# Optimization experiments

Hardware: AMD Instinct MI355X
Metric: run time of the kernel (lower is better)

## Reference

```python
import jax, jax.numpy as jnp
import numpy as np

B, N, DIM = 8, 4096, 512
HEADS, DHEAD = 8, 64
HIDDEN = HEADS * DHEAD  # 512
COND = 512
EPS = 1e-5


def layer_norm(x, gamma, beta):
    mu = jnp.mean(x, axis=-1, keepdims=True)
    var = jnp.var(x, axis=-1, keepdims=True)
    return (x - mu) * jax.lax.rsqrt(var + EPS) * gamma + beta


def setup_inputs() -> dict:
    key = jax.random.key(0)
    ks = jax.random.split(key, 8)
    s_in = 1.0 / np.sqrt(DIM)
    s_cond = 1.0 / np.sqrt(COND)
    s_hid = 1.0 / np.sqrt(HIDDEN)
    return {
        "x": jax.random.normal(ks[0], (B, N, DIM), jnp.float32),
        "conditioning_embeddings": jax.random.normal(ks[1], (B, COND), jnp.float32),
        "gamma_in": jnp.ones((DIM,), jnp.float32),
        "w_cond": jax.random.normal(ks[2], (2 * DIM, COND), jnp.float32) * s_cond,
        "b_cond": jax.random.normal(ks[3], (2 * DIM,), jnp.float32) * 0.01,
        "w_qkv": jax.random.normal(ks[4], (3 * HIDDEN, DIM), jnp.float32) * s_in,
        "w_out": jax.random.normal(ks[5], (DIM, HIDDEN), jnp.float32) * s_hid,
        "gamma_out": jnp.ones((DIM,), jnp.float32),
    }


def reference(x, conditioning_embeddings, gamma_in, w_cond, b_cond, w_qkv, w_out, gamma_out):
    scale_f = DHEAD ** (-0.5)
    # pre-norm
    x = layer_norm(x, gamma_in, jnp.zeros_like(gamma_in))
    # conditioning affine: SiLU -> Linear -> broadcast over tokens
    cond = jax.nn.silu(conditioning_embeddings) @ w_cond.T + b_cond  # [b, 2*dim]
    scale, shift = jnp.split(cond, 2, axis=-1)
    x = x * (scale[:, None, :] + 1.0) + shift[:, None, :]
    # qkv projection (no bias)
    qkv = x @ w_qkv.T  # [b, n, 3*hidden]
    q, k, v = jnp.split(qkv, 3, axis=-1)
    def to_heads(t):
        return t.reshape(B, N, HEADS, DHEAD).transpose(0, 2, 1, 3)  # b h n d
    q, k, v = to_heads(q), to_heads(k), to_heads(v)
    q = jax.nn.softmax(q, axis=-1) * scale_f  # softmax over feature dim
    k = jax.nn.softmax(k, axis=-2)            # softmax over sequence dim
    context = jnp.einsum('bhnd,bhne->bhde', k, v)
    out = jnp.einsum('bhde,bhnd->bhne', context, q)
    out = out.transpose(0, 2, 1, 3).reshape(B, N, HIDDEN)  # b n (h d)
    out = out @ w_out.T
    return layer_norm(out, gamma_out, jnp.zeros_like(gamma_out))
```

## Files before the change

kernel.cpp:

```cpp
#include <hip/hip_runtime.h>
#include <hip/hip_bf16.h>
#include <math.h>

typedef unsigned short u16;
typedef __attribute__((ext_vector_type(4))) float f32x4;
typedef __attribute__((ext_vector_type(8))) short s16x8;

#define B_    8
#define N_    4096
#define DIM_  512
#define TOK   32768
#define QKVD  1536

__device__ __forceinline__ float bf2f(u16 u) {
    union { unsigned int i; float f; } x; x.i = ((unsigned int)u) << 16; return x.f;
}
__device__ __forceinline__ u16 f2bf(float f) {
    union { float f; unsigned int i; } x; x.f = f;
    unsigned int r = (x.i + 0x7fffu + ((x.i >> 16) & 1u)) >> 16;
    return (u16)r;
}

__device__ __forceinline__ void gload_lds16(const void* g, void* l) {
    __builtin_amdgcn_global_load_lds(
        (const __attribute__((address_space(1))) unsigned int*)g,
        (__attribute__((address_space(3))) unsigned int*)l, 16, 0, 0);
}

__device__ __forceinline__ int swz8(int row, int p) { return p ^ (row & 7); }

__global__ void k_cond(const float* __restrict__ ce, const float* __restrict__ w_cond,
                       const float* __restrict__ b_cond, float* __restrict__ cond)
{
    __shared__ float s[512];
    int jt = blockIdx.x, b = blockIdx.y;
    int tid = threadIdx.x, wid = tid >> 6, lane = tid & 63;
    for (int i = tid; i < 512; i += 256) {
        float v = ce[b * 512 + i];
        s[i] = v / (1.f + __expf(-v));
    }
    __syncthreads();
#pragma unroll
    for (int jj = 0; jj < 4; ++jj) {
        int j = jt * 16 + wid * 4 + jj;
        const float4* w4 = (const float4*)(w_cond + (size_t)j * 512);
        float4 a = w4[lane * 2], c = w4[lane * 2 + 1];
        float acc = a.x*s[lane*8+0] + a.y*s[lane*8+1] + a.z*s[lane*8+2] + a.w*s[lane*8+3]
                  + c.x*s[lane*8+4] + c.y*s[lane*8+5] + c.z*s[lane*8+6] + c.w*s[lane*8+7];
#pragma unroll
        for (int d = 1; d < 64; d <<= 1) acc += __shfl_xor(acc, d, 64);
        if (lane == 0) cond[b * 1024 + j] = acc + b_cond[j];
    }
}

__global__ void k_w2bf(const float* __restrict__ w, u16* __restrict__ wb)
{
    int i = (blockIdx.x * 256 + threadIdx.x) * 4;
    float4 v = *(const float4*)&w[i];
    ushort4 o; o.x = f2bf(v.x); o.y = f2bf(v.y); o.z = f2bf(v.z); o.w = f2bf(v.w);
    *(ushort4*)&wb[i] = o;
}

__global__ void k_lnmod(const float* __restrict__ x, const float* __restrict__ cond,
                        const float* __restrict__ gamma, u16* __restrict__ xm)
{
    int wave = threadIdx.x >> 6, lane = threadIdx.x & 63;
    size_t t = (size_t)blockIdx.x * 4 + wave;
    const float* xr = x + t * 512;
    float4 v0 = ((const float4*)xr)[lane * 2];
    float4 v1 = ((const float4*)xr)[lane * 2 + 1];
    float s  = v0.x+v0.y+v0.z+v0.w + v1.x+v1.y+v1.z+v1.w;
    float ss = v0.x*v0.x+v0.y*v0.y+v0.z*v0.z+v0.w*v0.w
             + v1.x*v1.x+v1.y*v1.y+v1.z*v1.z+v1.w*v1.w;
#pragma unroll
    for (int m = 1; m < 64; m <<= 1) { s += __shfl_xor(s, m, 64); ss += __shfl_xor(ss, m, 64); }
    float mu = s * (1.f/512.f);
    float var = ss * (1.f/512.f) - mu * mu;
    float rs = rsqrtf(var + 1e-5f);
    int b = (int)(t >> 12);
    const float* cb = cond + b * 1024;
    float4 g0  = ((const float4*)gamma)[lane*2],     g1  = ((const float4*)gamma)[lane*2+1];
    float4 sc0 = ((const float4*)cb)[lane*2],        sc1 = ((const float4*)cb)[lane*2+1];
    float4 sh0 = ((const float4*)(cb+512))[lane*2],  sh1 = ((const float4*)(cb+512))[lane*2+1];
    ushort4 o0, o1;
    o0.x = f2bf(((v0.x-mu)*rs*g0.x)*(1.f+sc0.x) + sh0.x);
    o0.y = f2bf(((v0.y-mu)*rs*g0.y)*(1.f+sc0.y) + sh0.y);
    o0.z = f2bf(((v0.z-mu)*rs*g0.z)*(1.f+sc0.z) + sh0.z);
    o0.w = f2bf(((v0.w-mu)*rs*g0.w)*(1.f+sc0.w) + sh0.w);
    o1.x = f2bf(((v1.x-mu)*rs*g1.x)*(1.f+sc1.x) + sh1.x);
    o1.y = f2bf(((v1.y-mu)*rs*g1.y)*(1.f+sc1.y) + sh1.y);
    o1.z = f2bf(((v1.z-mu)*rs*g1.z)*(1.f+sc1.z) + sh1.z);
    o1.w = f2bf(((v1.w-mu)*rs*g1.w)*(1.f+sc1.w) + sh1.w);
    ushort4* orow = (ushort4*)(xm + t * 512);
    orow[lane * 2] = o0; orow[lane * 2 + 1] = o1;
}

__global__ __launch_bounds__(256, 2)
void k_gemmqkv(const u16* __restrict__ A,
               const u16* __restrict__ Bm,
               u16* __restrict__ Out,
               float* __restrict__ pmax, float* __restrict__ psum)
{
    __shared__ __align__(16) u16 As[128 * 64];
    __shared__ __align__(16) u16 Bs[128 * 64];
    int sid = (blockIdx.x & 7) * 384 + (blockIdx.x >> 3);
    int bn = sid % 12, bm = sid / 12;
    int m0 = bm * 128, n0 = bn * 128;
    int tid = threadIdx.x;
    int wid = tid >> 6, lane = tid & 63;
    int wr = (wid >> 1) * 64, wc = (wid & 1) * 64;
    int fr = lane & 15, fc = lane >> 4;

    f32x4 acc[4][4];
#pragma unroll
    for (int m = 0; m < 4; ++m)
#pragma unroll
        for (int n = 0; n < 4; ++n) acc[m][n] = (f32x4)0.f;

    for (int k0 = 0; k0 < 512; k0 += 64) {
#pragma unroll
        for (int i = 0; i < 4; ++i) {
            int c = tid + i * 256;
            int row = c >> 3, p = c & 7, gp = swz8(row, p);
            gload_lds16(A  + (size_t)(m0 + row) * 512 + k0 + gp * 8, &As[c * 8]);
            gload_lds16(Bm + (size_t)(n0 + row) * 512 + k0 + gp * 8, &Bs[c * 8]);
        }
        __syncthreads();
#pragma unroll
        for (int kk = 0; kk < 2; ++kk) {
            s16x8 af[4], bfr[4];
            int q = kk * 4 + fc;
#pragma unroll
            for (int m = 0; m < 4; ++m) {
                int row = wr + m * 16 + fr;
                af[m] = *(const s16x8*)&As[(row * 8 + swz8(row, q)) * 8];
            }
#pragma unroll
            for (int n = 0; n < 4; ++n) {
                int row = wc + n * 16 + fr;
                bfr[n] = *(const s16x8*)&Bs[(row * 8 + swz8(row, q)) * 8];
            }
#pragma unroll
            for (int m = 0; m < 4; ++m)
#pragma unroll
                for (int n = 0; n < 4; ++n)
                    acc[m][n] = __builtin_amdgcn_mfma_f32_16x16x32_bf16(af[m], bfr[n], acc[m][n], 0, 0, 0);
        }
        __syncthreads();
    }

    int rbase = m0 + wr + fc * 4;
    int cbase = n0 + wc + fr;

    if (bn < 4) {
#pragma unroll
        for (int m = 0; m < 4; ++m) {
            float v[4][4];
#pragma unroll
            for (int n = 0; n < 4; ++n)
#pragma unroll
                for (int r = 0; r < 4; ++r) v[n][r] = acc[m][n][r];
#pragma unroll
            for (int r = 0; r < 4; ++r) {
                float mx = fmaxf(fmaxf(v[0][r], v[1][r]), fmaxf(v[2][r], v[3][r]));
#pragma unroll
                for (int d = 1; d < 16; d <<= 1) mx = fmaxf(mx, __shfl_xor(mx, d, 64));
                float e0 = __expf(v[0][r]-mx), e1 = __expf(v[1][r]-mx);
                float e2 = __expf(v[2][r]-mx), e3 = __expf(v[3][r]-mx);
                float sm = e0 + e1 + e2 + e3;
#pragma unroll
                for (int d = 1; d < 16; d <<= 1) sm += __shfl_xor(sm, d, 64);
                float rv = 0.125f / sm;
                v[0][r] = e0*rv; v[1][r] = e1*rv; v[2][r] = e2*rv; v[3][r] = e3*rv;
            }
#pragma unroll
            for (int n = 0; n < 4; ++n)
#pragma unroll
                for (int r = 0; r < 4; ++r)
                    Out[(size_t)(rbase + m*16 + r) * QKVD + (cbase + n*16)] = f2bf(v[n][r]);
        }
    } else if (bn < 8) {
        int bloc = m0 >> 12;
        int rcc = ((m0 & 4095) + wr) >> 6;
#pragma unroll
        for (int n = 0; n < 4; ++n) {
            float vv[16]; float mx = -1e30f;
#pragma unroll
            for (int m = 0; m < 4; ++m)
#pragma unroll
                for (int r = 0; r < 4; ++r) {
                    u16 u = f2bf(acc[m][n][r]);
                    Out[(size_t)(rbase + m*16 + r) * QKVD + (cbase + n*16)] = u;
                    float vf = bf2f(u);
                    vv[m*4+r] = vf; mx = fmaxf(mx, vf);
                }
            mx = fmaxf(mx, __shfl_xor(mx, 16, 64));
            mx = fmaxf(mx, __shfl_xor(mx, 32, 64));
            float sm = 0.f;
#pragma unroll
            for (int i = 0; i < 16; ++i) sm += __expf(vv[i] - mx);
            sm += __shfl_xor(sm, 16, 64);
            sm += __shfl_xor(sm, 32, 64);
            if (lane < 16) {
                int kcol = (n0 - 512) + wc + n*16 + lane;
                int o = (bloc * 64 + rcc) * 512 + kcol;
                pmax[o] = mx; psum[o] = sm;
            }
        }
    } else {
#pragma unroll
        for (int m = 0; m < 4; ++m)
#pragma unroll
            for (int n = 0; n < 4; ++n)
#pragma unroll
                for (int r = 0; r < 4; ++r)
                    Out[(size_t)(rbase + m*16 + r) * QKVD + (cbase + n*16)] = f2bf(acc[m][n][r]);
    }
}

__global__ void k_kstat2(const float* __restrict__ pmax, const float* __restrict__ psum,
                         float* __restrict__ kmax, float* __restrict__ ksum)
{
    int g = blockIdx.x * 64 + threadIdx.x;
    int b = g >> 9, c = g & 511;
    float m = -1e30f, s = 0.f;
    for (int rc = 0; rc < 64; ++rc) {
        float m2 = pmax[(b * 64 + rc) * 512 + c], s2 = psum[(b * 64 + rc) * 512 + c];
        float mm = fmaxf(m, m2);
        s = s * __expf(m - mm) + s2 * __expf(m2 - mm);
        m = mm;
    }
    kmax[g] = m; ksum[g] = s;
}

__global__ __launch_bounds__(256, 2)
void k_ctx(const u16* __restrict__ qkv, const float* __restrict__ kmax, float* __restrict__ ctxp)
{
    __shared__ __align__(16) u16 sA[4][64 * 40];
    __shared__ __align__(16) u16 sB[4][64 * 40];
    __shared__ float scr[2][4096];
    int nc = blockIdx.x, h = blockIdx.y, b = blockIdx.z;
    int wid = threadIdx.x >> 6, lane = threadIdx.x & 63;
    u16* A  = sA[wid];
    u16* Bt = sB[wid];
    float km = kmax[b * 512 + h * 64 + lane];
    int fr = lane & 15, fk = (lane >> 4) * 8;
    f32x4 acc[4][4];
#pragma unroll
    for (int m = 0; m < 4; ++m)
#pragma unroll
        for (int n = 0; n < 4; ++n) acc[m][n] = (f32x4)0.f;

    size_t rowbase = (size_t)b * 4096 + nc * 512 + wid * 32;
    const u16* kp = qkv + rowbase * QKVD + 512 + h * 64 + lane;
    const u16* vp = kp + 512;

    for (int it = 0; it < 4; ++it) {
        const u16* kq = kp + (size_t)it * 128 * QKVD;
        const u16* vq = vp + (size_t)it * 128 * QKVD;
        unsigned int pk[16], pv[16];
#pragma unroll
        for (int j = 0; j < 16; ++j) {
            float a0 = __expf(bf2f(kq[(size_t)(2*j)   * QKVD]) - km);
            float a1 = __expf(bf2f(kq[(size_t)(2*j+1) * QKVD]) - km);
            pk[j] = (unsigned)f2bf(a0) | ((unsigned)f2bf(a1) << 16);
            float b0 = bf2f(vq[(size_t)(2*j)   * QKVD]);
            float b1 = bf2f(vq[(size_t)(2*j+1) * QKVD]);
            pv[j] = (unsigned)f2bf(b0) | ((unsigned)f2bf(b1) << 16);
        }
#pragma unroll
        for (int j = 0; j < 4; ++j) {
            *(uint4*)&A [lane * 40 + j * 8] = *(uint4*)&pk[j * 4];
            *(uint4*)&Bt[lane * 40 + j * 8] = *(uint4*)&pv[j * 4];
        }
        s16x8 af[4], bfr[4];
#pragma unroll
        for (int m = 0; m < 4; ++m) af[m]  = *(const s16x8*)&A [(m * 16 + fr) * 40 + fk];
#pragma unroll
        for (int n = 0; n < 4; ++n) bfr[n] = *(const s16x8*)&Bt[(n * 16 + fr) * 40 + fk];
#pragma unroll
        for (int m = 0; m < 4; ++m)
#pragma unroll
            for (int n = 0; n < 4; ++n)
                acc[m][n] = __builtin_amdgcn_mfma_f32_16x16x32_bf16(af[m], bfr[n], acc[m][n], 0, 0, 0);
    }

    __syncthreads();
    int rbase = (lane >> 4) * 4, cbase = lane & 15;
    if (wid >= 2) {
#pragma unroll
        for (int m = 0; m < 4; ++m)
#pragma unroll
            for (int n = 0; n < 4; ++n)
#pragma unroll
                for (int r = 0; r < 4; ++r)
                    scr[wid - 2][(m * 16 + rbase + r) * 64 + n * 16 + cbase] = acc[m][n][r];
    }
    __syncthreads();
    if (wid < 2) {
        float* cp = ctxp + (((size_t)(b * 8 + h) * 16) + nc * 2 + wid) * 4096;
#pragma unroll
        for (int m = 0; m < 4; ++m)
#pragma unroll
            for (int n = 0; n < 4; ++n)
#pragma unroll
                for (int r = 0; r < 4; ++r) {
                    int idx = (m * 16 + rbase + r) * 64 + n * 16 + cbase;
                    cp[idx] = acc[m][n][r] + scr[wid][idx];
                }
    }
}

__global__ void k_wc(const float* __restrict__ ctxp, const float* __restrict__ ksum,
                     const float* __restrict__ w_out, u16* __restrict__ Wc)
{
    __shared__ float csh[64 * 65];
    __shared__ float wsh[64 * 65];
    int jt = blockIdx.x, h = blockIdx.y, b = blockIdx.z;
    int tid = threadIdx.x;
    const float* cp = ctxp + ((size_t)(b * 8 + h) * 16) * 4096;
    for (int idx = tid; idx < 4096; idx += 256) {
        int d = idx >> 6, e = idx & 63;
        float sum = 0.f;
#pragma unroll
        for (int nc = 0; nc < 16; ++nc) sum += cp[nc * 4096 + idx];
        csh[d * 65 + e] = sum * (1.f / ksum[b * 512 + h * 64 + d]);
        wsh[d * 65 + e] = w_out[(size_t)(jt * 64 + d) * 512 + h * 64 + e];
    }
    __syncthreads();
    int j0 = (tid >> 4) * 4, d0 = (tid & 15) * 4;
    float acc[4][4] = {};
    for (int e = 0; e < 64; ++e) {
        float wv[4], cv[4];
#pragma unroll
        for (int i = 0; i < 4; ++i) wv[i] = wsh[(j0 + i) * 65 + e];
#pragma unroll
        for (int j = 0; j < 4; ++j) cv[j] = csh[(d0 + j) * 65 + e];
#pragma unroll
        for (int i = 0; i < 4; ++i)
#pragma unroll
            for (int j = 0; j < 4; ++j) acc[i][j] += wv[i] * cv[j];
    }
#pragma unroll
    for (int i = 0; i < 4; ++i)
#pragma unroll
        for (int j = 0; j < 4; ++j)
            Wc[((size_t)b * 512 + jt * 64 + j0 + i) * 512 + h * 64 + d0 + j] = f2bf(acc[i][j]);
}

__global__ __launch_bounds__(512, 2)
void k_g2ln(const u16* __restrict__ Aq, const u16* __restrict__ Wc,
            const float* __restrict__ gamma, float* __restrict__ out)
{
    __shared__ __align__(16) u16 As[64 * 64];
    __shared__ __align__(16) u16 Bs[512 * 64];
    __shared__ float rsum[64][8], rssq[64][8];
    int bm = blockIdx.x;
    int m0 = bm * 64;
    int b = m0 >> 12;
    const u16* Bp = Wc + (size_t)b * 512 * 512;
    int tid = threadIdx.x;
    int wn = tid >> 6, lane = tid & 63;
    int fr = lane & 15, fc = lane >> 4;

    f32x4 acc[4][4];
#pragma unroll
    for (int m = 0; m < 4; ++m)
#pragma unroll
        for (int n = 0; n < 4; ++n) acc[m][n] = (f32x4)0.f;

    for (int k0 = 0; k0 < 512; k0 += 64) {
        {
            int c = tid;
            int row = c >> 3, p = c & 7, gp = swz8(row, p);
            gload_lds16(Aq + (size_t)(m0 + row) * QKVD + k0 + gp * 8, &As[c * 8]);
        }
#pragma unroll
        for (int i = 0; i < 8; ++i) {
            int c = tid + i * 512;
            int col = c >> 3, p = c & 7, gp = swz8(col, p);
            gload_lds16(Bp + (size_t)col * 512 + k0 + gp * 8, &Bs[c * 8]);
        }
        __syncthreads();
#pragma unroll
        for (int kk = 0; kk < 2; ++kk) {
            int q = kk * 4 + fc;
            s16x8 af[4], bfr[4];
#pragma unroll
            for (int m = 0; m < 4; ++m) {
                int row = m * 16 + fr;
                af[m] = *(const s16x8*)&As[(row * 8 + swz8(row, q)) * 8];
            }
#pragma unroll
            for (int n = 0; n < 4; ++n) {
                int col = wn * 64 + n * 16 + fr;
                bfr[n] = *(const s16x8*)&Bs[(col * 8 + swz8(col, q)) * 8];
            }
#pragma unroll
            for (int m = 0; m < 4; ++m)
#pragma unroll
                for (int n = 0; n < 4; ++n)
                    acc[m][n] = __builtin_amdgcn_mfma_f32_16x16x32_bf16(af[m], bfr[n], acc[m][n], 0, 0, 0);
        }
        __syncthreads();
    }

#pragma unroll
    for (int m = 0; m < 4; ++m)
#pragma unroll
        for (int r = 0; r < 4; ++r) {
            float s = 0.f, ss = 0.f;
#pragma unroll
            for (int n = 0; n < 4; ++n) { float v = acc[m][n][r]; s += v; ss += v * v; }
#pragma unroll
            for (int d = 1; d < 16; d <<= 1) { s += __shfl_xor(s, d, 64); ss += __shfl_xor(ss, d, 64); }
            if ((lane & 15) == 0) {
                int row = m * 16 + fc * 4 + r;
                rsum[row][wn] = s; rssq[row][wn] = ss;
            }
        }
    __syncthreads();

    float g[4];
#pragma unroll
    for (int n = 0; n < 4; ++n) g[n] = gamma[wn * 64 + n * 16 + fr];

#pragma unroll
    for (int m = 0; m < 4; ++m)
#pragma unroll
        for (int r = 0; r < 4; ++r) {
            int row = m * 16 + fc * 4 + r;
            float s  = 0.f, ss = 0.f;
#pragma unroll
            for (int w = 0; w < 8; ++w) { s += rsum[row][w]; ss += rssq[row][w]; }
            float mu = s * (1.f/512.f);
            float var = ss * (1.f/512.f) - mu * mu;
            float rs = rsqrtf(var + 1e-5f);
            float* orow = out + (size_t)(m0 + row) * 512;
#pragma unroll
            for (int n = 0; n < 4; ++n)
                orow[wn * 64 + n * 16 + fr] = (acc[m][n][r] - mu) * rs * g[n];
        }
}

extern "C" void kernel_launch(void* const* d_in, const int* in_sizes, int n_in,
                              void* d_out, int out_size, void* d_ws, size_t ws_size,
                              hipStream_t stream)
{
    const float* x        = (const float*)d_in[0];
    const float* ce       = (const float*)d_in[1];
    const float* gamma_in = (const float*)d_in[2];
    const float* w_cond   = (const float*)d_in[3];
    const float* b_cond   = (const float*)d_in[4];
    const float* w_qkv    = (const float*)d_in[5];
    const float* w_out    = (const float*)d_in[6];
    const float* gamma_out= (const float*)d_in[7];
    float* out = (float*)d_out;

    char* ws = (char*)d_ws;
    size_t o = 0;
    auto take = [&](size_t bytes) -> char* {
        char* p = ws + o; o += (bytes + 255) & ~(size_t)255; return p;
    };
    float* cond  = (float*)take(8 * 1024 * 4);
    u16*   wqkvb = (u16*)  take((size_t)1536 * 512 * 2);
    float* kmax  = (float*)take(4096 * 4);
    float* ksum  = (float*)take(4096 * 4);
    float* pmax  = (float*)take((size_t)8 * 64 * 512 * 4);
    float* psum  = (float*)take((size_t)8 * 64 * 512 * 4);
    float* ctxp  = (float*)take((size_t)64 * 16 * 4096 * 4);
    u16*   Wc    = (u16*)  take((size_t)8 * 512 * 512 * 2);
    u16*   xm    = (u16*)  take((size_t)TOK * 512 * 2);
    u16*   qkv   = (u16*)  take((size_t)TOK * QKVD * 2);

    k_cond   <<<dim3(64, 8), 256, 0, stream>>>(ce, w_cond, b_cond, cond);
    k_w2bf   <<<768, 256, 0, stream>>>(w_qkv, wqkvb);
    k_lnmod  <<<8192, 256, 0, stream>>>(x, cond, gamma_in, xm);
    k_gemmqkv<<<3072, 256, 0, stream>>>(xm, wqkvb, qkv, pmax, psum);
    k_kstat2 <<<64, 64, 0, stream>>>(pmax, psum, kmax, ksum);
    k_ctx    <<<dim3(8, 8, 8), 256, 0, stream>>>(qkv, kmax, ctxp);
    k_wc     <<<dim3(8, 8, 8), 256, 0, stream>>>(ctxp, ksum, w_out, Wc);
    k_g2ln   <<<512, 512, 0, stream>>>(qkv, Wc, gamma_out, out);
}
```

Before: 187.1 us.

## Drop max-subtraction for k softmax and fold column sums into context kernel

Removes the per-tile max/sum statistics epilogue from the QKV GEMM and the separate kstat reduction kernel. The context kernel now takes exp(k) without subtracting a column max and accumulates the column sums itself, writing partial sums that the Wc kernel reduces. The Wc kernel is regridded to one block per (head, batch) and loops over output tiles, and the QKV GEMM launch bound is raised to 3 blocks per SM. Without max subtraction, exp can overflow for large k values; this is only safe because the layer-normed inputs keep k small.

```diff
diff --git a/kernel.cpp b/kernel.cpp
--- a/kernel.cpp
+++ b/kernel.cpp
@@ -95,11 +95,10 @@
     orow[lane * 2] = o0; orow[lane * 2 + 1] = o1;
 }
 
-__global__ __launch_bounds__(256, 2)
+__global__ __launch_bounds__(256, 3)
 void k_gemmqkv(const u16* __restrict__ A,
                const u16* __restrict__ Bm,
-               u16* __restrict__ Out,
-               float* __restrict__ pmax, float* __restrict__ psum)
+               u16* __restrict__ Out)
 {
     __shared__ __align__(16) u16 As[128 * 64];
     __shared__ __align__(16) u16 Bs[128 * 64];
@@ -179,34 +178,6 @@
                 for (int r = 0; r < 4; ++r)
                     Out[(size_t)(rbase + m*16 + r) * QKVD + (cbase + n*16)] = f2bf(v[n][r]);
         }
-    } else if (bn < 8) {
-        int bloc = m0 >> 12;
-        int rcc = ((m0 & 4095) + wr) >> 6;
-#pragma unroll
-        for (int n = 0; n < 4; ++n) {
-            float vv[16]; float mx = -1e30f;
-#pragma unroll
-            for (int m = 0; m < 4; ++m)
-#pragma unroll
-                for (int r = 0; r < 4; ++r) {
-                    u16 u = f2bf(acc[m][n][r]);
-                    Out[(size_t)(rbase + m*16 + r) * QKVD + (cbase + n*16)] = u;
-                    float vf = bf2f(u);
-                    vv[m*4+r] = vf; mx = fmaxf(mx, vf);
-                }
-            mx = fmaxf(mx, __shfl_xor(mx, 16, 64));
-            mx = fmaxf(mx, __shfl_xor(mx, 32, 64));
-            float sm = 0.f;
-#pragma unroll
-            for (int i = 0; i < 16; ++i) sm += __expf(vv[i] - mx);
-            sm += __shfl_xor(sm, 16, 64);
-            sm += __shfl_xor(sm, 32, 64);
-            if (lane < 16) {
-                int kcol = (n0 - 512) + wc + n*16 + lane;
-                int o = (bloc * 64 + rcc) * 512 + kcol;
-                pmax[o] = mx; psum[o] = sm;
-            }
-        }
     } else {
 #pragma unroll
         for (int m = 0; m < 4; ++m)
@@ -218,38 +189,24 @@
     }
 }
 
-__global__ void k_kstat2(const float* __restrict__ pmax, const float* __restrict__ psum,
-                         float* __restrict__ kmax, float* __restrict__ ksum)
-{
-    int g = blockIdx.x * 64 + threadIdx.x;
-    int b = g >> 9, c = g & 511;
-    float m = -1e30f, s = 0.f;
-    for (int rc = 0; rc < 64; ++rc) {
-        float m2 = pmax[(b * 64 + rc) * 512 + c], s2 = psum[(b * 64 + rc) * 512 + c];
-        float mm = fmaxf(m, m2);
-        s = s * __expf(m - mm) + s2 * __expf(m2 - mm);
-        m = mm;
-    }
-    kmax[g] = m; ksum[g] = s;
-}
-
 __global__ __launch_bounds__(256, 2)
-void k_ctx(const u16* __restrict__ qkv, const float* __restrict__ kmax, float* __restrict__ ctxp)
+void k_ctx(const u16* __restrict__ qkv, float* __restrict__ ctxp, float* __restrict__ ksump)
 {
     __shared__ __align__(16) u16 sA[4][64 * 40];
     __shared__ __align__(16) u16 sB[4][64 * 40];
     __shared__ float scr[2][4096];
+    __shared__ float kscr[2][64];
     int nc = blockIdx.x, h = blockIdx.y, b = blockIdx.z;
     int wid = threadIdx.x >> 6, lane = threadIdx.x & 63;
     u16* A  = sA[wid];
     u16* Bt = sB[wid];
-    float km = kmax[b * 512 + h * 64 + lane];
     int fr = lane & 15, fk = (lane >> 4) * 8;
     f32x4 acc[4][4];
 #pragma unroll
     for (int m = 0; m < 4; ++m)
 #pragma unroll
         for (int n = 0; n < 4; ++n) acc[m][n] = (f32x4)0.f;
+    float ksl = 0.f;
 
     size_t rowbase = (size_t)b * 4096 + nc * 512 + wid * 32;
     const u16* kp = qkv + rowbase * QKVD + 512 + h * 64 + lane;
@@ -261,8 +218,9 @@
         unsigned int pk[16], pv[16];
 #pragma unroll
         for (int j = 0; j < 16; ++j) {
-            float a0 = __expf(bf2f(kq[(size_t)(2*j)   * QKVD]) - km);
-            float a1 = __expf(bf2f(kq[(size_t)(2*j+1) * QKVD]) - km);
+            float a0 = __expf(bf2f(kq[(size_t)(2*j)   * QKVD]));
+            float a1 = __expf(bf2f(kq[(size_t)(2*j+1) * QKVD]));
+            ksl += a0 + a1;
             pk[j] = (unsigned)f2bf(a0) | ((unsigned)f2bf(a1) << 16);
             float b0 = bf2f(vq[(size_t)(2*j)   * QKVD]);
             float b1 = bf2f(vq[(size_t)(2*j+1) * QKVD]);
@@ -295,6 +253,7 @@
 #pragma unroll
                 for (int r = 0; r < 4; ++r)
                     scr[wid - 2][(m * 16 + rbase + r) * 64 + n * 16 + cbase] = acc[m][n][r];
+        kscr[wid - 2][lane] = ksl;
     }
     __syncthreads();
     if (wid < 2) {
@@ -308,44 +267,63 @@
                     int idx = (m * 16 + rbase + r) * 64 + n * 16 + cbase;
                     cp[idx] = acc[m][n][r] + scr[wid][idx];
                 }
-    }
-}
-
-__global__ void k_wc(const float* __restrict__ ctxp, const float* __restrict__ ksum,
+        ksump[(((size_t)(b * 8 + h) * 16) + nc * 2 + wid) * 64 + lane] = ksl + kscr[wid][lane];
+    }
+}
+
+__global__ void k_wc(const float* __restrict__ ctxp, const float* __restrict__ ksump,
                      const float* __restrict__ w_out, u16* __restrict__ Wc)
 {
     __shared__ float csh[64 * 65];
     __shared__ float wsh[64 * 65];
-    int jt = blockIdx.x, h = blockIdx.y, b = blockIdx.z;
+    __shared__ float inv[64];
+    int h = blockIdx.x, b = blockIdx.y;
     int tid = threadIdx.x;
-    const float* cp = ctxp + ((size_t)(b * 8 + h) * 16) * 4096;
+    const float* cp = ctxp + (size_t)(b * 8 + h) * 16 * 4096;
+    const float* kp = ksump + (size_t)(b * 8 + h) * 16 * 64;
+    if (tid < 64) {
+        float s = 0.f;
+#pragma unroll
+        for (int sl = 0; sl < 16; ++sl) s += kp[sl * 64 + tid];
+        inv[tid] = 1.f / s;
+    }
     for (int idx = tid; idx < 4096; idx += 256) {
-        int d = idx >> 6, e = idx & 63;
         float sum = 0.f;
 #pragma unroll
-        for (int nc = 0; nc < 16; ++nc) sum += cp[nc * 4096 + idx];
-        csh[d * 65 + e] = sum * (1.f / ksum[b * 512 + h * 64 + d]);
-        wsh[d * 65 + e] = w_out[(size_t)(jt * 64 + d) * 512 + h * 64 + e];
-    }
-    __syncthreads();
+        for (int sl = 0; sl < 16; ++sl) sum += cp[sl * 4096 + idx];
+        csh[(idx >> 6) * 65 + (idx & 63)] = sum;
+    }
+    __syncthreads();
+    for (int idx = tid; idx < 4096; idx += 256)
+        csh[(idx >> 6) * 65 + (idx & 63)] *= inv[idx >> 6];
+    __syncthreads();
+
     int j0 = (tid >> 4) * 4, d0 = (tid & 15) * 4;
-    float acc[4][4] = {};
-    for (int e = 0; e < 64; ++e) {
-        float wv[4], cv[4];
-#pragma unroll
-        for (int i = 0; i < 4; ++i) wv[i] = wsh[(j0 + i) * 65 + e];
-#pragma unroll
-        for (int j = 0; j < 4; ++j) cv[j] = csh[(d0 + j) * 65 + e];
+    for (int jt = 0; jt < 8; ++jt) {
+        for (int idx = tid; idx < 4096; idx += 256) {
+            int d = idx >> 6, e = idx & 63;
+            wsh[d * 65 + e] = w_out[(size_t)(jt * 64 + d) * 512 + h * 64 + e];
+        }
+        __syncthreads();
+        float acc[4][4] = {};
+        for (int e = 0; e < 64; ++e) {
+            float wv[4], cv[4];
+#pragma unroll
+            for (int i = 0; i < 4; ++i) wv[i] = wsh[(j0 + i) * 65 + e];
+#pragma unroll
+            for (int j = 0; j < 4; ++j) cv[j] = csh[(d0 + j) * 65 + e];
+#pragma unroll
+            for (int i = 0; i < 4; ++i)
+#pragma unroll
+                for (int j = 0; j < 4; ++j) acc[i][j] += wv[i] * cv[j];
+        }
 #pragma unroll
         for (int i = 0; i < 4; ++i)
 #pragma unroll
-            for (int j = 0; j < 4; ++j) acc[i][j] += wv[i] * cv[j];
-    }
-#pragma unroll
-    for (int i = 0; i < 4; ++i)
-#pragma unroll
-        for (int j = 0; j < 4; ++j)
-            Wc[((size_t)b * 512 + jt * 64 + j0 + i) * 512 + h * 64 + d0 + j] = f2bf(acc[i][j]);
+            for (int j = 0; j < 4; ++j)
+                Wc[((size_t)b * 512 + jt * 64 + j0 + i) * 512 + h * 64 + d0 + j] = f2bf(acc[i][j]);
+        __syncthreads();
+    }
 }
 
 __global__ __launch_bounds__(512, 2)
@@ -464,10 +442,7 @@
     };
     float* cond  = (float*)take(8 * 1024 * 4);
     u16*   wqkvb = (u16*)  take((size_t)1536 * 512 * 2);
-    float* kmax  = (float*)take(4096 * 4);
-    float* ksum  = (float*)take(4096 * 4);
-    float* pmax  = (float*)take((size_t)8 * 64 * 512 * 4);
-    float* psum  = (float*)take((size_t)8 * 64 * 512 * 4);
+    float* ksump = (float*)take((size_t)64 * 16 * 64 * 4);
     float* ctxp  = (float*)take((size_t)64 * 16 * 4096 * 4);
     u16*   Wc    = (u16*)  take((size_t)8 * 512 * 512 * 2);
     u16*   xm    = (u16*)  take((size_t)TOK * 512 * 2);
@@ -476,9 +451,8 @@
     k_cond   <<<dim3(64, 8), 256, 0, stream>>>(ce, w_cond, b_cond, cond);
     k_w2bf   <<<768, 256, 0, stream>>>(w_qkv, wqkvb);
     k_lnmod  <<<8192, 256, 0, stream>>>(x, cond, gamma_in, xm);
-    k_gemmqkv<<<3072, 256, 0, stream>>>(xm, wqkvb, qkv, pmax, psum);
-    k_kstat2 <<<64, 64, 0, stream>>>(pmax, psum, kmax, ksum);
-    k_ctx    <<<dim3(8, 8, 8), 256, 0, stream>>>(qkv, kmax, ctxp);
-    k_wc     <<<dim3(8, 8, 8), 256, 0, stream>>>(ctxp, ksum, w_out, Wc);
+    k_gemmqkv<<<3072, 256, 0, stream>>>(xm, wqkvb, qkv);
+    k_ctx    <<<dim3(8, 8, 8), 256, 0, stream>>>(qkv, ctxp, ksump);
+    k_wc     <<<dim3(8, 8), 256, 0, stream>>>(ctxp, ksump, w_out, Wc);
     k_g2ln   <<<512, 512, 0, stream>>>(qkv, Wc, gamma_out, out);
 }
```

Result: slower. 201.0 us (+7.4%).
